# Kernel optimization log

Measured on AMD Instinct MI355X. Metric: run time of the kernel, lower is better.

The kernel has to match this reference:

```python
import jax, jax.numpy as jnp
import numpy as np

N = 50000      # nodes
F_IN = 1024    # raw feature dim
D = 64         # student_dim = hidden_dim * compression_ratio
P = 3          # number of meta-paths
E = 1600000    # edges per meta-path adjacency (avg degree 32)


def setup_inputs() -> dict:
    key = jax.random.key(0)
    ks = jax.random.split(key, 10)
    feats = jax.random.normal(ks[0], (N, F_IN), jnp.float32)
    rows = jax.random.randint(ks[1], (P, E), 0, N, dtype=jnp.int32)
    cols = jax.random.randint(ks[2], (P, E), 0, N, dtype=jnp.int32)
    # normalized-adjacency-like positive edge weights
    vals = jax.random.uniform(ks[3], (P, E), jnp.float32) / 32.0
    # fc_list[0]: Linear(F_IN -> D), xavier_normal gain=1.414
    W0 = jax.random.normal(ks[4], (D, F_IN), jnp.float32) * 0.05
    b0 = jnp.zeros((D,), jnp.float32)
    # P GCN linear layers (D -> D, no bias) + GCN bias params
    Wg = jax.random.normal(ks[5], (P, D, D), jnp.float32) * 0.17
    bg = jnp.zeros((P, D), jnp.float32)
    # PReLU alpha (torch default init 0.25, one scalar per GCN)
    alpha = jnp.full((P,), 0.25, jnp.float32)
    # Attention: Linear(D -> D) and att vector [1, D]
    Wa = jax.random.normal(ks[6], (D, D), jnp.float32) * 0.17
    ba = jnp.zeros((D,), jnp.float32)
    att = jax.random.normal(ks[7], (1, D), jnp.float32) * 0.17
    return dict(feats=feats, rows=rows, cols=cols, vals=vals, W0=W0, b0=b0,
                Wg=Wg, bg=bg, alpha=alpha, Wa=Wa, ba=ba, att=att)


def reference(feats, rows, cols, vals, W0, b0, Wg, bg, alpha, Wa, ba, att):
    # h = elu(fc_list[0](feats))  (feat_drop = 0 -> identity)
    h = jax.nn.elu(feats @ W0.T + b0)                       # [N, D]
    embeds = []
    for i in range(P):
        s = h @ Wg[i].T                                     # [N, D]
        # sparse adj (COO) @ s : out[r] += v * s[c]
        msg = vals[i][:, None] * s[cols[i]]                 # [E, D]
        out = jax.ops.segment_sum(msg, rows[i], num_segments=N)
        out = out + bg[i]
        embeds.append(jnp.where(out > 0, out, alpha[i] * out))  # PReLU
    emb = jnp.stack(embeds)                                 # [P, N, D]
    # Attention over views: beta_i = att . mean_n tanh(fc(emb_i))
    sp = jnp.tanh(jnp.einsum('pnd,ed->pne', emb, Wa) + ba).mean(axis=1)  # [P, D]
    beta = jax.nn.softmax(sp @ att[0])                      # [P]
    z_mp = jnp.einsum('p,pnd->nd', beta, emb)               # [N, D]
    return z_mp
```

## Files before the change

kernel.cpp:

```cpp
#include <hip/hip_runtime.h>
#include <hip/hip_bf16.h>

#define N_NODES 50000
#define F_IN    1024
#define DD      64
#define PP      3
#define EE      1600000
#define NPC     98
#define CCAP    17664

typedef __attribute__((ext_vector_type(8))) short short8v;
typedef __attribute__((ext_vector_type(4))) float floatx4;
typedef __attribute__((ext_vector_type(2))) float floatx2;

__device__ inline float bfl(uint u) { return __uint_as_float(u << 16); }
__device__ inline float bfh(uint u) { return __uint_as_float(u & 0xffff0000u); }
__device__ inline floatx2 up2(uint u) {
    floatx2 r; r.x = bfl(u); r.y = bfh(u); return r;
}
__device__ inline uint cvtpk2(float a, float b) {
    __hip_bfloat162 h = __float22bfloat162_rn(make_float2(a, b));
    return *(uint*)&h;
}
__device__ inline ushort f2bf(float x) {
    __hip_bfloat16 h = __float2bfloat16(x);
    return *(ushort*)&h;
}

__global__ __launch_bounds__(256) void split_weights(const float* __restrict__ W0,
                                                     const float* __restrict__ Wg,
                                                     ushort* __restrict__ W0h,
                                                     ushort* __restrict__ Wgh)
{
    int i = blockIdx.x * 256 + threadIdx.x;
    if (i < 64 * 1024) W0h[i] = f2bf(W0[i]);
    int j = i - 64 * 1024;
    if (j >= 0 && j < PP * 64 * 64) Wgh[j] = f2bf(Wg[j]);
}

__global__ __launch_bounds__(256) void gemm1_fused(const float* __restrict__ feats,
                                                   const ushort* __restrict__ W0h,
                                                   const float* __restrict__ b0,
                                                   const ushort* __restrict__ Wgh,
                                                   ushort* __restrict__ s_all)
{
    __shared__ ushort Ah[64 * 64];
    __shared__ ushort Bh[64 * 64];
    const int t = threadIdx.x;
    const int w = t >> 6, lane = t & 63;
    const int row0 = blockIdx.x * 64;
    const int l15 = lane & 15, l4 = lane >> 4;

    floatx4 acc[4] = {};

    for (int kc = 0; kc < 16; ++kc) {
        #pragma unroll
        for (int rep = 0; rep < 4; ++rep) {
            int idx = rep * 256 + t;
            int r = idx >> 4, c4 = idx & 15;
            int gr = row0 + r; if (gr >= N_NODES) gr = N_NODES - 1;
            float4 v = *(const float4*)&feats[(size_t)gr * F_IN + kc * 64 + c4 * 4];
            int unit = (c4 >> 1) ^ (r & 7);
            int base = r * 64 + unit * 8 + (c4 & 1) * 4;
            *(uint2*)&Ah[base] = make_uint2(cvtpk2(v.x, v.y), cvtpk2(v.z, v.w));
        }
        #pragma unroll
        for (int rep = 0; rep < 2; ++rep) {
            int idx = rep * 256 + t;
            int c = idx >> 3, u8 = idx & 7;
            uint4 vh = *(const uint4*)&W0h[(size_t)c * F_IN + kc * 64 + u8 * 8];
            int unit = u8 ^ (c & 7);
            *(uint4*)&Bh[c * 64 + unit * 8] = vh;
        }
        __syncthreads();
        #pragma unroll
        for (int ks = 0; ks < 2; ++ks) {
            int arow = w * 16 + l15;
            int au = (ks * 4 + l4) ^ (arow & 7);
            short8v ah = *(short8v*)&Ah[arow * 64 + au * 8];
            #pragma unroll
            for (int cf = 0; cf < 4; ++cf) {
                int bcol = cf * 16 + l15;
                int bu = (ks * 4 + l4) ^ (bcol & 7);
                short8v bh = *(short8v*)&Bh[bcol * 64 + bu * 8];
                acc[cf] = __builtin_amdgcn_mfma_f32_16x16x32_bf16(ah, bh, acc[cf], 0, 0, 0);
            }
        }
        __syncthreads();
    }

    #pragma unroll
    for (int cf = 0; cf < 4; ++cf) {
        int col = cf * 16 + l15;
        #pragma unroll
        for (int r = 0; r < 4; ++r) {
            int row = w * 16 + l4 * 4 + r;
            float x = acc[cf][r] + b0[col];
            x = x > 0.f ? x : (__expf(x) - 1.f);
            int u = (col >> 3) ^ (row & 7);
            Ah[row * 64 + u * 8 + (col & 7)] = f2bf(x);
        }
    }
    __syncthreads();

    for (int p = 0; p < PP; ++p) {
        #pragma unroll
        for (int rep = 0; rep < 2; ++rep) {
            int idx = rep * 256 + t;
            int r = idx >> 3, u8 = idx & 7;
            int unit = u8 ^ (r & 7);
            *(uint4*)&Bh[r * 64 + unit * 8] = *(const uint4*)&Wgh[(size_t)p * 4096 + idx * 8];
        }
        __syncthreads();

        floatx4 sacc[4] = {};
        #pragma unroll
        for (int ks = 0; ks < 2; ++ks) {
            int arow = w * 16 + l15;
            int au = (ks * 4 + l4) ^ (arow & 7);
            short8v ah = *(short8v*)&Ah[arow * 64 + au * 8];
            #pragma unroll
            for (int cf = 0; cf < 4; ++cf) {
                int bcol = cf * 16 + l15;
                int bu = (ks * 4 + l4) ^ (bcol & 7);
                short8v bh = *(short8v*)&Bh[bcol * 64 + bu * 8];
                sacc[cf] = __builtin_amdgcn_mfma_f32_16x16x32_bf16(ah, bh, sacc[cf], 0, 0, 0);
            }
        }
        ushort* sp = s_all + (size_t)p * N_NODES * 64;
        #pragma unroll
        for (int cf = 0; cf < 4; ++cf) {
            int col = cf * 16 + l15;
            #pragma unroll
            for (int r = 0; r < 4; ++r) {
                int gr = row0 + w * 16 + l4 * 4 + r;
                if (gr < N_NODES)
                    sp[(size_t)gr * 64 + col] = f2bf(sacc[cf][r]);
            }
        }
        __syncthreads();
    }
}

__global__ __launch_bounds__(256) void part1(const int*   __restrict__ rows,
                                             const int*   __restrict__ cols,
                                             const float* __restrict__ vals,
                                             int*   __restrict__ pcur3,
                                             uint2* __restrict__ coarsebuf)
{
    __shared__ uint2 stage[2560];
    __shared__ uint2 sorted[2560];
    __shared__ int cnt[128];
    __shared__ int sc[128];
    __shared__ int curb[128];
    __shared__ int gbase[128];
    const int t = threadIdx.x;
    const int path = blockIdx.y;
    const size_t ebase = (size_t)path * EE + (size_t)blockIdx.x * 2560;
    int* pcur = pcur3 + path * NPC;
    uint2* cb = coarsebuf + (size_t)path * NPC * CCAP;

    if (t < 128) { cnt[t] = 0; curb[t] = 0; }
    __syncthreads();

    #pragma unroll
    for (int it = 0; it < 10; ++it) {
        int e = it * 256 + t;
        int r = rows[ebase + e];
        int c = cols[ebase + e];
        float v = vals[ebase + e];
        int bin = r >> 9, rl = r & 511;
        stage[e] = make_uint2((uint)c | ((uint)rl << 16) | ((uint)bin << 25),
                              __float_as_uint(v));
        atomicAdd(&cnt[bin], 1);
    }
    __syncthreads();

    if (t < 128) sc[t] = cnt[t];
    __syncthreads();
    #pragma unroll
    for (int o = 1; o < 128; o <<= 1) {
        int v = (t < 128 && t >= o) ? sc[t - o] : 0;
        __syncthreads();
        if (t < 128 && t >= o) sc[t] += v;
        __syncthreads();
    }

    if (t < NPC) gbase[t] = atomicAdd(&pcur[t], cnt[t]);
    __syncthreads();

    #pragma unroll
    for (int it = 0; it < 10; ++it) {
        uint2 e = stage[it * 256 + t];
        int bin = e.x >> 25;
        int loc = (sc[bin] - cnt[bin]) + atomicAdd(&curb[bin], 1);
        sorted[loc] = e;
    }
    __syncthreads();

    #pragma unroll
    for (int it = 0; it < 10; ++it) {
        int i = it * 256 + t;
        uint2 e = sorted[i];
        int bin = e.x >> 25;
        int g = gbase[bin] + (i - (sc[bin] - cnt[bin]));
        if (g < CCAP) cb[(size_t)bin * CCAP + g] = e;
    }
}

__global__ __launch_bounds__(512) void sort2(const uint2* __restrict__ coarsebuf,
                                             const int*   __restrict__ pcur3,
                                             uint* __restrict__ sortpk,
                                             int* __restrict__ rowbeg3,
                                             int* __restrict__ rowend3)
{
    __shared__ int hist[512];
    __shared__ int cur[512];
    const int t = threadIdx.x;
    const int c = blockIdx.x, path = blockIdx.y;
    const int n = min(pcur3[path * NPC + c], CCAP);
    const size_t slabbase = ((size_t)path * NPC + c) * CCAP;
    const uint2* src = coarsebuf + slabbase;

    hist[t] = 0;
    __syncthreads();

    for (int i = t; i < n; i += 512)
        atomicAdd(&hist[(src[i].x >> 16) & 511], 1);
    __syncthreads();

    int c0 = hist[t];
    __syncthreads();
    #pragma unroll
    for (int o = 1; o < 512; o <<= 1) {
        int v = (t >= o) ? hist[t - o] : 0;
        __syncthreads();
        hist[t] += v;
        __syncthreads();
    }
    int excl = hist[t] - c0;
    cur[t] = excl;
    int gr = c * 512 + t;
    if (gr < N_NODES) {
        rowbeg3[path * N_NODES + gr] = (int)(slabbase + excl);
        rowend3[path * N_NODES + gr] = (int)(slabbase + excl + c0);
    }
    __syncthreads();

    for (int i = t; i < n; i += 512) {
        uint2 e = src[i];
        int rl = (e.x >> 16) & 511;
        int pos = atomicAdd(&cur[rl], 1);
        sortpk[slabbase + pos] = (e.x & 0xffffu) |
                                 ((uint)f2bf(__uint_as_float(e.y)) << 16);
    }
}

__global__ __launch_bounds__(256) void spmm_gather(const uint*   __restrict__ sortpk,
                                                   const int*    __restrict__ rowbeg3,
                                                   const int*    __restrict__ rowend3,
                                                   const ushort* __restrict__ s_all,
                                                   const float*  __restrict__ bg,
                                                   const float*  __restrict__ alpha,
                                                   ushort* __restrict__ emb)
{
    const int path = blockIdx.x / 12500;
    const int wid = (blockIdx.x % 12500) * 4 + (threadIdx.x >> 6);
    const int lane = threadIdx.x & 63;
    const int dq = lane & 7;
    const int slot = lane >> 3;
    const int e0 = rowbeg3[path * N_NODES + wid];
    const int e1 = rowend3[path * N_NODES + wid];
    const ushort* s_p = s_all + (size_t)path * N_NODES * 64;

    floatx2 acc[4] = {};
    if (e0 < e1) {
        const int last = e1 - 1;
        for (int e = e0; e < e1; e += 32) {
            int ea = e + slot, eb = ea + 8, ec = ea + 16, ed = ea + 24;
            uint pka = sortpk[min(ea, last)];
            uint pkb = sortpk[min(eb, last)];
            uint pkc = sortpk[min(ec, last)];
            uint pkd = sortpk[min(ed, last)];
            const uint4 ga = *(const uint4*)&s_p[(size_t)(pka & 0xffffu) * 64 + dq * 8];
            const uint4 gb = *(const uint4*)&s_p[(size_t)(pkb & 0xffffu) * 64 + dq * 8];
            const uint4 gc = *(const uint4*)&s_p[(size_t)(pkc & 0xffffu) * 64 + dq * 8];
            const uint4 gd = *(const uint4*)&s_p[(size_t)(pkd & 0xffffu) * 64 + dq * 8];
            float va = (ea <= last) ? bfh(pka) : 0.f;
            float vb = (eb <= last) ? bfh(pkb) : 0.f;
            float vc = (ec <= last) ? bfh(pkc) : 0.f;
            float vd = (ed <= last) ? bfh(pkd) : 0.f;
            floatx2 va2 = {va, va}, vb2 = {vb, vb}, vc2 = {vc, vc}, vd2 = {vd, vd};
            acc[0] += va2 * up2(ga.x); acc[1] += va2 * up2(ga.y);
            acc[2] += va2 * up2(ga.z); acc[3] += va2 * up2(ga.w);
            acc[0] += vb2 * up2(gb.x); acc[1] += vb2 * up2(gb.y);
            acc[2] += vb2 * up2(gb.z); acc[3] += vb2 * up2(gb.w);
            acc[0] += vc2 * up2(gc.x); acc[1] += vc2 * up2(gc.y);
            acc[2] += vc2 * up2(gc.z); acc[3] += vc2 * up2(gc.w);
            acc[0] += vd2 * up2(gd.x); acc[1] += vd2 * up2(gd.y);
            acc[2] += vd2 * up2(gd.z); acc[3] += vd2 * up2(gd.w);
        }
    }
    #pragma unroll
    for (int j = 0; j < 4; ++j) {
        acc[j].x += __shfl_xor(acc[j].x, 8);
        acc[j].y += __shfl_xor(acc[j].y, 8);
        acc[j].x += __shfl_xor(acc[j].x, 16);
        acc[j].y += __shfl_xor(acc[j].y, 16);
        acc[j].x += __shfl_xor(acc[j].x, 32);
        acc[j].y += __shfl_xor(acc[j].y, 32);
    }

    if (slot == 0) {
        const float al = alpha[path];
        const float* bgp = bg + path * 64;
        float x[8];
        #pragma unroll
        for (int j = 0; j < 4; ++j) {
            float v0 = acc[j].x + bgp[dq * 8 + 2 * j];
            float v1 = acc[j].y + bgp[dq * 8 + 2 * j + 1];
            x[2 * j]     = v0 > 0.f ? v0 : al * v0;
            x[2 * j + 1] = v1 > 0.f ? v1 : al * v1;
        }
        uint4 wv;
        wv.x = cvtpk2(x[0], x[1]);
        wv.y = cvtpk2(x[2], x[3]);
        wv.z = cvtpk2(x[4], x[5]);
        wv.w = cvtpk2(x[6], x[7]);
        *(uint4*)&emb[((size_t)path * N_NODES + wid) * 64 + dq * 8] = wv;
    }
}

__global__ __launch_bounds__(256) void postproc(const ushort* __restrict__ emb,
                                                const float* __restrict__ Wa,
                                                const float* __restrict__ ba,
                                                float* __restrict__ sp)
{
    __shared__ float Ws[64][64];
    __shared__ float As[64][64];
    __shared__ float red[16][64];
    const int t  = threadIdx.x;
    const int tx = t & 15;
    const int ty = t >> 4;
    const int nb = (N_NODES + 63) >> 6;
    const int p  = blockIdx.x / nb;
    const int tb = blockIdx.x % nb;
    const int row0 = tb * 64;
    const ushort* embp = emb + (size_t)p * N_NODES * 64;

    #pragma unroll
    for (int rep = 0; rep < 4; ++rep) {
        int id = rep * 1024 + t * 4;
        int e  = id >> 6;
        int k4 = id & 63;
        float4 wv = *(const float4*)&Wa[id];
        Ws[k4+0][e] = wv.x; Ws[k4+1][e] = wv.y;
        Ws[k4+2][e] = wv.z; Ws[k4+3][e] = wv.w;
    }
    #pragma unroll
    for (int rep = 0; rep < 2; ++rep) {
        int idx = rep * 256 + t;
        int m  = idx >> 3;
        int d8 = idx & 7;
        int gr = row0 + m;
        int gr2 = gr < N_NODES ? gr : N_NODES - 1;
        uint4 xv = *(const uint4*)&embp[(size_t)gr2 * 64 + d8 * 8];
        As[d8*8+0][m] = bfl(xv.x); As[d8*8+1][m] = bfh(xv.x);
        As[d8*8+2][m] = bfl(xv.y); As[d8*8+3][m] = bfh(xv.y);
        As[d8*8+4][m] = bfl(xv.z); As[d8*8+5][m] = bfh(xv.z);
        As[d8*8+6][m] = bfl(xv.w); As[d8*8+7][m] = bfh(xv.w);
    }
    __syncthreads();

    float acc[4][4] = {};
    #pragma unroll 8
    for (int kk = 0; kk < 64; ++kk) {
        float4 a4 = *(const float4*)&As[kk][ty * 4];
        float4 b4 = *(const float4*)&Ws[kk][tx * 4];
        float av[4] = {a4.x, a4.y, a4.z, a4.w};
        float bv[4] = {b4.x, b4.y, b4.z, b4.w};
        #pragma unroll
        for (int i = 0; i < 4; ++i)
            #pragma unroll
            for (int j = 0; j < 4; ++j)
                acc[i][j] += av[i] * bv[j];
    }

    float colsum[4] = {0.f, 0.f, 0.f, 0.f};
    #pragma unroll
    for (int i = 0; i < 4; ++i) {
        int gr = row0 + ty * 4 + i;
        if (gr < N_NODES) {
            #pragma unroll
            for (int j = 0; j < 4; ++j)
                colsum[j] += tanhf(acc[i][j] + ba[tx * 4 + j]);
        }
    }
    #pragma unroll
    for (int j = 0; j < 4; ++j) red[ty][tx * 4 + j] = colsum[j];
    __syncthreads();
    if (t < 64) {
        float ssum = 0.f;
        #pragma unroll
        for (int g = 0; g < 16; ++g) ssum += red[g][t];
        unsafeAtomicAdd(&sp[p * 64 + t], ssum);
    }
}

__global__ void beta_kernel(const float* __restrict__ sp,
                            const float* __restrict__ att,
                            float* __restrict__ beta)
{
    int lane = threadIdx.x;
    float w[PP];
    #pragma unroll
    for (int p = 0; p < PP; ++p) {
        float x = sp[p * 64 + lane] * (1.0f / (float)N_NODES) * att[lane];
        #pragma unroll
        for (int off = 32; off; off >>= 1) x += __shfl_down(x, off);
        w[p] = __shfl(x, 0);
    }
    if (lane == 0) {
        float mx = fmaxf(w[0], fmaxf(w[1], w[2]));
        float e0 = __expf(w[0] - mx);
        float e1 = __expf(w[1] - mx);
        float e2 = __expf(w[2] - mx);
        float s = e0 + e1 + e2;
        beta[0] = e0 / s; beta[1] = e1 / s; beta[2] = e2 / s;
    }
}

__global__ __launch_bounds__(256) void combine(const ushort* __restrict__ emb,
                                               const float* __restrict__ beta,
                                               float* __restrict__ out)
{
    const float b0 = beta[0], b1 = beta[1], b2 = beta[2];
    const size_t tot = (size_t)N_NODES * 64;
    size_t i = ((size_t)blockIdx.x * 256 + threadIdx.x) * 8;
    if (i < tot) {
        uint4 e0 = *(const uint4*)&emb[i];
        uint4 e1 = *(const uint4*)&emb[tot + i];
        uint4 e2 = *(const uint4*)&emb[2 * tot + i];
        float o[8];
        o[0] = b0*bfl(e0.x) + b1*bfl(e1.x) + b2*bfl(e2.x);
        o[1] = b0*bfh(e0.x) + b1*bfh(e1.x) + b2*bfh(e2.x);
        o[2] = b0*bfl(e0.y) + b1*bfl(e1.y) + b2*bfl(e2.y);
        o[3] = b0*bfh(e0.y) + b1*bfh(e1.y) + b2*bfh(e2.y);
        o[4] = b0*bfl(e0.z) + b1*bfl(e1.z) + b2*bfl(e2.z);
        o[5] = b0*bfh(e0.z) + b1*bfh(e1.z) + b2*bfh(e2.z);
        o[6] = b0*bfl(e0.w) + b1*bfl(e1.w) + b2*bfl(e2.w);
        o[7] = b0*bfh(e0.w) + b1*bfh(e1.w) + b2*bfh(e2.w);
        *(float4*)&out[i]     = make_float4(o[0], o[1], o[2], o[3]);
        *(float4*)&out[i + 4] = make_float4(o[4], o[5], o[6], o[7]);
    }
}

extern "C" void kernel_launch(void* const* d_in, const int* in_sizes, int n_in,
                              void* d_out, int out_size, void* d_ws, size_t ws_size,
                              hipStream_t stream)
{
    const float* feats = (const float*)d_in[0];
    const int*   rows  = (const int*)  d_in[1];
    const int*   cols  = (const int*)  d_in[2];
    const float* vals  = (const float*)d_in[3];
    const float* W0    = (const float*)d_in[4];
    const float* b0    = (const float*)d_in[5];
    const float* Wg    = (const float*)d_in[6];
    const float* bg    = (const float*)d_in[7];
    const float* alpha = (const float*)d_in[8];
    const float* Wa    = (const float*)d_in[9];
    const float* ba    = (const float*)d_in[10];
    const float* att   = (const float*)d_in[11];
    float* out = (float*)d_out;

    const size_t ND = (size_t)N_NODES * 64;
    char* base = (char*)d_ws;
    ushort* emb    = (ushort*)base;              base += 3 * ND * 2;
    ushort* s_all  = (ushort*)base;              base += 3 * ND * 2;
    ushort* W0h    = (ushort*)base;              base += 64 * 1024 * 2;
    ushort* Wgh    = (ushort*)base;              base += PP * 64 * 64 * 2;
    int*    pcur3  = (int*)base;                 base += PP * NPC * 4;
    float*  sp     = (float*)base;               base += 192 * 4;
    float*  beta   = (float*)base;               base += 64 * 4;
    int*    rowbeg3 = (int*)base;                base += PP * N_NODES * 4;
    int*    rowend3 = (int*)base;                base += PP * N_NODES * 4;
    base = (char*)(((size_t)base + 255) & ~(size_t)255);
    uint2*  coarsebuf = (uint2*)base;            base += (size_t)PP * NPC * CCAP * 8;
    uint*   sortpk    = (uint*)base;             base += (size_t)PP * NPC * CCAP * 4;

    hipMemsetAsync(pcur3, 0, (PP * NPC + 192) * sizeof(int), stream);

    split_weights<<<(64 * 1024 + PP * 64 * 64 + 255) / 256, 256, 0, stream>>>(
        W0, Wg, W0h, Wgh);

    gemm1_fused<<<782, 256, 0, stream>>>(feats, W0h, b0, Wgh, s_all);

    part1<<<dim3(EE / 2560, 3), 256, 0, stream>>>(rows, cols, vals, pcur3, coarsebuf);
    sort2<<<dim3(NPC, 3), 512, 0, stream>>>(coarsebuf, pcur3, sortpk, rowbeg3, rowend3);
    spmm_gather<<<3 * 12500, 256, 0, stream>>>(
        sortpk, rowbeg3, rowend3, s_all, bg, alpha, emb);

    postproc<<<3 * 782, 256, 0, stream>>>(emb, Wa, ba, sp);
    beta_kernel<<<1, 64, 0, stream>>>(sp, att, beta);
    combine<<<(int)((ND / 8 + 255) / 256), 256, 0, stream>>>(emb, beta, out);
}
```

Baseline: 313.4 us.

## Map eight rows per wave in SpMM gather and prefetch GEMM tiles into registers

The SpMM gather kernel now gives each wave eight rows, with one 8-lane group per row, instead of one row per wave. This removes the cross-lane shuffle reduction and cuts the block count, at the cost of divergence when rows in a wave have different degrees; the loop runs until every group is done. Separately, the first GEMM register-prefetches the next K-chunk of feats and W0 while the MFMAs run on the current one, overlapping global loads with compute at some register cost.

```diff
diff --git a/kernel.cpp b/kernel.cpp
--- a/kernel.cpp
+++ b/kernel.cpp
@@ -8,6 +8,7 @@
 #define EE      1600000
 #define NPC     98
 #define CCAP    17664
+#define RG      1563
 
 typedef __attribute__((ext_vector_type(8))) short short8v;
 typedef __attribute__((ext_vector_type(4))) float floatx4;
@@ -52,27 +53,58 @@
     const int l15 = lane & 15, l4 = lane >> 4;
 
     floatx4 acc[4] = {};
+    float4 pa[4];
+    uint4  pb[2];
+
+    #pragma unroll
+    for (int rep = 0; rep < 4; ++rep) {
+        int idx = rep * 256 + t;
+        int r = idx >> 4, c4 = idx & 15;
+        int gr = row0 + r; if (gr >= N_NODES) gr = N_NODES - 1;
+        pa[rep] = *(const float4*)&feats[(size_t)gr * F_IN + c4 * 4];
+    }
+    #pragma unroll
+    for (int rep = 0; rep < 2; ++rep) {
+        int idx = rep * 256 + t;
+        int c = idx >> 3, u8 = idx & 7;
+        pb[rep] = *(const uint4*)&W0h[(size_t)c * F_IN + u8 * 8];
+    }
 
     for (int kc = 0; kc < 16; ++kc) {
         #pragma unroll
         for (int rep = 0; rep < 4; ++rep) {
             int idx = rep * 256 + t;
             int r = idx >> 4, c4 = idx & 15;
-            int gr = row0 + r; if (gr >= N_NODES) gr = N_NODES - 1;
-            float4 v = *(const float4*)&feats[(size_t)gr * F_IN + kc * 64 + c4 * 4];
             int unit = (c4 >> 1) ^ (r & 7);
             int base = r * 64 + unit * 8 + (c4 & 1) * 4;
-            *(uint2*)&Ah[base] = make_uint2(cvtpk2(v.x, v.y), cvtpk2(v.z, v.w));
+            *(uint2*)&Ah[base] = make_uint2(cvtpk2(pa[rep].x, pa[rep].y),
+                                            cvtpk2(pa[rep].z, pa[rep].w));
         }
         #pragma unroll
         for (int rep = 0; rep < 2; ++rep) {
             int idx = rep * 256 + t;
             int c = idx >> 3, u8 = idx & 7;
-            uint4 vh = *(const uint4*)&W0h[(size_t)c * F_IN + kc * 64 + u8 * 8];
             int unit = u8 ^ (c & 7);
-            *(uint4*)&Bh[c * 64 + unit * 8] = vh;
-        }
-        __syncthreads();
+            *(uint4*)&Bh[c * 64 + unit * 8] = pb[rep];
+        }
+        __syncthreads();
+
+        if (kc < 15) {
+            #pragma unroll
+            for (int rep = 0; rep < 4; ++rep) {
+                int idx = rep * 256 + t;
+                int r = idx >> 4, c4 = idx & 15;
+                int gr = row0 + r; if (gr >= N_NODES) gr = N_NODES - 1;
+                pa[rep] = *(const float4*)&feats[(size_t)gr * F_IN + (kc + 1) * 64 + c4 * 4];
+            }
+            #pragma unroll
+            for (int rep = 0; rep < 2; ++rep) {
+                int idx = rep * 256 + t;
+                int c = idx >> 3, u8 = idx & 7;
+                pb[rep] = *(const uint4*)&W0h[(size_t)c * F_IN + (kc + 1) * 64 + u8 * 8];
+            }
+        }
+
         #pragma unroll
         for (int ks = 0; ks < 2; ++ks) {
             int arow = w * 16 + l15;
@@ -264,54 +296,49 @@
                                                    const float*  __restrict__ alpha,
                                                    ushort* __restrict__ emb)
 {
-    const int path = blockIdx.x / 12500;
-    const int wid = (blockIdx.x % 12500) * 4 + (threadIdx.x >> 6);
+    const int path = blockIdx.x / RG;
+    const int bi   = blockIdx.x % RG;
+    const int wv   = threadIdx.x >> 6;
     const int lane = threadIdx.x & 63;
-    const int dq = lane & 7;
-    const int slot = lane >> 3;
-    const int e0 = rowbeg3[path * N_NODES + wid];
-    const int e1 = rowend3[path * N_NODES + wid];
+    const int g    = lane >> 3;
+    const int dq   = lane & 7;
+    const int row  = (bi * 4 + wv) * 8 + g;
+    const int rowc = min(row, N_NODES - 1);
+    const int e0   = rowbeg3[path * N_NODES + rowc];
+    const int e1   = rowend3[path * N_NODES + rowc];
+    const int last = max(e1 - 1, 0);
     const ushort* s_p = s_all + (size_t)path * N_NODES * 64;
 
     floatx2 acc[4] = {};
-    if (e0 < e1) {
-        const int last = e1 - 1;
-        for (int e = e0; e < e1; e += 32) {
-            int ea = e + slot, eb = ea + 8, ec = ea + 16, ed = ea + 24;
-            uint pka = sortpk[min(ea, last)];
-            uint pkb = sortpk[min(eb, last)];
-            uint pkc = sortpk[min(ec, last)];
-            uint pkd = sortpk[min(ed, last)];
-            const uint4 ga = *(const uint4*)&s_p[(size_t)(pka & 0xffffu) * 64 + dq * 8];
-            const uint4 gb = *(const uint4*)&s_p[(size_t)(pkb & 0xffffu) * 64 + dq * 8];
-            const uint4 gc = *(const uint4*)&s_p[(size_t)(pkc & 0xffffu) * 64 + dq * 8];
-            const uint4 gd = *(const uint4*)&s_p[(size_t)(pkd & 0xffffu) * 64 + dq * 8];
-            float va = (ea <= last) ? bfh(pka) : 0.f;
-            float vb = (eb <= last) ? bfh(pkb) : 0.f;
-            float vc = (ec <= last) ? bfh(pkc) : 0.f;
-            float vd = (ed <= last) ? bfh(pkd) : 0.f;
-            floatx2 va2 = {va, va}, vb2 = {vb, vb}, vc2 = {vc, vc}, vd2 = {vd, vd};
-            acc[0] += va2 * up2(ga.x); acc[1] += va2 * up2(ga.y);
-            acc[2] += va2 * up2(ga.z); acc[3] += va2 * up2(ga.w);
-            acc[0] += vb2 * up2(gb.x); acc[1] += vb2 * up2(gb.y);
-            acc[2] += vb2 * up2(gb.z); acc[3] += vb2 * up2(gb.w);
-            acc[0] += vc2 * up2(gc.x); acc[1] += vc2 * up2(gc.y);
-            acc[2] += vc2 * up2(gc.z); acc[3] += vc2 * up2(gc.w);
-            acc[0] += vd2 * up2(gd.x); acc[1] += vd2 * up2(gd.y);
-            acc[2] += vd2 * up2(gd.z); acc[3] += vd2 * up2(gd.w);
-        }
-    }
-    #pragma unroll
-    for (int j = 0; j < 4; ++j) {
-        acc[j].x += __shfl_xor(acc[j].x, 8);
-        acc[j].y += __shfl_xor(acc[j].y, 8);
-        acc[j].x += __shfl_xor(acc[j].x, 16);
-        acc[j].y += __shfl_xor(acc[j].y, 16);
-        acc[j].x += __shfl_xor(acc[j].x, 32);
-        acc[j].y += __shfl_xor(acc[j].y, 32);
-    }
-
-    if (slot == 0) {
+    for (int e = e0; __any(e < e1); e += 4) {
+        int i0 = min(e,     last);
+        int i1 = min(e + 1, last);
+        int i2 = min(e + 2, last);
+        int i3 = min(e + 3, last);
+        uint pk0 = sortpk[i0];
+        uint pk1 = sortpk[i1];
+        uint pk2 = sortpk[i2];
+        uint pk3 = sortpk[i3];
+        const uint4 g0 = *(const uint4*)&s_p[(size_t)(pk0 & 0xffffu) * 64 + dq * 8];
+        const uint4 g1 = *(const uint4*)&s_p[(size_t)(pk1 & 0xffffu) * 64 + dq * 8];
+        const uint4 g2 = *(const uint4*)&s_p[(size_t)(pk2 & 0xffffu) * 64 + dq * 8];
+        const uint4 g3 = *(const uint4*)&s_p[(size_t)(pk3 & 0xffffu) * 64 + dq * 8];
+        float v0 = (e     < e1) ? bfh(pk0) : 0.f;
+        float v1 = (e + 1 < e1) ? bfh(pk1) : 0.f;
+        float v2 = (e + 2 < e1) ? bfh(pk2) : 0.f;
+        float v3 = (e + 3 < e1) ? bfh(pk3) : 0.f;
+        floatx2 v02 = {v0, v0}, v12 = {v1, v1}, v22 = {v2, v2}, v32 = {v3, v3};
+        acc[0] += v02 * up2(g0.x); acc[1] += v02 * up2(g0.y);
+        acc[2] += v02 * up2(g0.z); acc[3] += v02 * up2(g0.w);
+        acc[0] += v12 * up2(g1.x); acc[1] += v12 * up2(g1.y);
+        acc[2] += v12 * up2(g1.z); acc[3] += v12 * up2(g1.w);
+        acc[0] += v22 * up2(g2.x); acc[1] += v22 * up2(g2.y);
+        acc[2] += v22 * up2(g2.z); acc[3] += v22 * up2(g2.w);
+        acc[0] += v32 * up2(g3.x); acc[1] += v32 * up2(g3.y);
+        acc[2] += v32 * up2(g3.z); acc[3] += v32 * up2(g3.w);
+    }
+
+    if (row < N_NODES) {
         const float al = alpha[path];
         const float* bgp = bg + path * 64;
         float x[8];
@@ -322,12 +349,12 @@
             x[2 * j]     = v0 > 0.f ? v0 : al * v0;
             x[2 * j + 1] = v1 > 0.f ? v1 : al * v1;
         }
-        uint4 wv;
-        wv.x = cvtpk2(x[0], x[1]);
-        wv.y = cvtpk2(x[2], x[3]);
-        wv.z = cvtpk2(x[4], x[5]);
-        wv.w = cvtpk2(x[6], x[7]);
-        *(uint4*)&emb[((size_t)path * N_NODES + wid) * 64 + dq * 8] = wv;
+        uint4 wvv;
+        wvv.x = cvtpk2(x[0], x[1]);
+        wvv.y = cvtpk2(x[2], x[3]);
+        wvv.z = cvtpk2(x[4], x[5]);
+        wvv.w = cvtpk2(x[6], x[7]);
+        *(uint4*)&emb[((size_t)path * N_NODES + row) * 64 + dq * 8] = wvv;
     }
 }
 
@@ -497,7 +524,7 @@
 
     part1<<<dim3(EE / 2560, 3), 256, 0, stream>>>(rows, cols, vals, pcur3, coarsebuf);
     sort2<<<dim3(NPC, 3), 512, 0, stream>>>(coarsebuf, pcur3, sortpk, rowbeg3, rowend3);
-    spmm_gather<<<3 * 12500, 256, 0, stream>>>(
+    spmm_gather<<<3 * RG, 256, 0, stream>>>(
         sortpk, rowbeg3, rowend3, s_all, bg, alpha, emb);
 
     postproc<<<3 * 782, 256, 0, stream>>>(emb, Wa, ba, sp);
```

Measured after the change: 322.3 us. 1.03x slower.

## Prefetch next K-tile in gemm1 and move attention GEMM onto bf16 MFMA

Applied to the files above, without the earlier changes.

gemm1_fused now loads the next K-chunk of feats and W0 into registers before the MFMA work of the current chunk, so global-load latency overlaps compute. The postproc attention projection moves from a scalar fp32 outer-product loop to bf16 MFMA with swizzled LDS tiles, and Wa is pre-converted to bf16 in split_weights. Feeding Wa in bf16 lowers the precision of the tanh scores, and the register prefetch raises register pressure.

```diff
diff --git a/kernel.cpp b/kernel.cpp
--- a/kernel.cpp
+++ b/kernel.cpp
@@ -29,13 +29,17 @@
 
 __global__ __launch_bounds__(256) void split_weights(const float* __restrict__ W0,
                                                      const float* __restrict__ Wg,
+                                                     const float* __restrict__ Wa,
                                                      ushort* __restrict__ W0h,
-                                                     ushort* __restrict__ Wgh)
+                                                     ushort* __restrict__ Wgh,
+                                                     ushort* __restrict__ Wah)
 {
     int i = blockIdx.x * 256 + threadIdx.x;
     if (i < 64 * 1024) W0h[i] = f2bf(W0[i]);
     int j = i - 64 * 1024;
     if (j >= 0 && j < PP * 64 * 64) Wgh[j] = f2bf(Wg[j]);
+    int k = i - 64 * 1024 - PP * 64 * 64;
+    if (k >= 0 && k < 64 * 64) Wah[k] = f2bf(Wa[k]);
 }
 
 __global__ __launch_bounds__(256) void gemm1_fused(const float* __restrict__ feats,
@@ -52,27 +56,58 @@
     const int l15 = lane & 15, l4 = lane >> 4;
 
     floatx4 acc[4] = {};
+    float4 pa[4];
+    uint4  pb[2];
+
+    #pragma unroll
+    for (int rep = 0; rep < 4; ++rep) {
+        int idx = rep * 256 + t;
+        int r = idx >> 4, c4 = idx & 15;
+        int gr = row0 + r; if (gr >= N_NODES) gr = N_NODES - 1;
+        pa[rep] = *(const float4*)&feats[(size_t)gr * F_IN + c4 * 4];
+    }
+    #pragma unroll
+    for (int rep = 0; rep < 2; ++rep) {
+        int idx = rep * 256 + t;
+        int c = idx >> 3, u8 = idx & 7;
+        pb[rep] = *(const uint4*)&W0h[(size_t)c * F_IN + u8 * 8];
+    }
 
     for (int kc = 0; kc < 16; ++kc) {
         #pragma unroll
         for (int rep = 0; rep < 4; ++rep) {
             int idx = rep * 256 + t;
             int r = idx >> 4, c4 = idx & 15;
-            int gr = row0 + r; if (gr >= N_NODES) gr = N_NODES - 1;
-            float4 v = *(const float4*)&feats[(size_t)gr * F_IN + kc * 64 + c4 * 4];
             int unit = (c4 >> 1) ^ (r & 7);
             int base = r * 64 + unit * 8 + (c4 & 1) * 4;
-            *(uint2*)&Ah[base] = make_uint2(cvtpk2(v.x, v.y), cvtpk2(v.z, v.w));
+            *(uint2*)&Ah[base] = make_uint2(cvtpk2(pa[rep].x, pa[rep].y),
+                                            cvtpk2(pa[rep].z, pa[rep].w));
         }
         #pragma unroll
         for (int rep = 0; rep < 2; ++rep) {
             int idx = rep * 256 + t;
             int c = idx >> 3, u8 = idx & 7;
-            uint4 vh = *(const uint4*)&W0h[(size_t)c * F_IN + kc * 64 + u8 * 8];
             int unit = u8 ^ (c & 7);
-            *(uint4*)&Bh[c * 64 + unit * 8] = vh;
-        }
-        __syncthreads();
+            *(uint4*)&Bh[c * 64 + unit * 8] = pb[rep];
+        }
+        __syncthreads();
+
+        if (kc < 15) {
+            #pragma unroll
+            for (int rep = 0; rep < 4; ++rep) {
+                int idx = rep * 256 + t;
+                int r = idx >> 4, c4 = idx & 15;
+                int gr = row0 + r; if (gr >= N_NODES) gr = N_NODES - 1;
+                pa[rep] = *(const float4*)&feats[(size_t)gr * F_IN + (kc + 1) * 64 + c4 * 4];
+            }
+            #pragma unroll
+            for (int rep = 0; rep < 2; ++rep) {
+                int idx = rep * 256 + t;
+                int c = idx >> 3, u8 = idx & 7;
+                pb[rep] = *(const uint4*)&W0h[(size_t)c * F_IN + (kc + 1) * 64 + u8 * 8];
+            }
+        }
+
         #pragma unroll
         for (int ks = 0; ks < 2; ++ks) {
             int arow = w * 16 + l15;
@@ -332,16 +367,16 @@
 }
 
 __global__ __launch_bounds__(256) void postproc(const ushort* __restrict__ emb,
-                                                const float* __restrict__ Wa,
+                                                const ushort* __restrict__ Wah,
                                                 const float* __restrict__ ba,
                                                 float* __restrict__ sp)
 {
-    __shared__ float Ws[64][64];
-    __shared__ float As[64][64];
+    __shared__ ushort Ah[64 * 64];
+    __shared__ ushort Bh[64 * 64];
     __shared__ float red[16][64];
-    const int t  = threadIdx.x;
-    const int tx = t & 15;
-    const int ty = t >> 4;
+    const int t = threadIdx.x;
+    const int w = t >> 6, lane = t & 63;
+    const int l15 = lane & 15, l4 = lane >> 4;
     const int nb = (N_NODES + 63) >> 6;
     const int p  = blockIdx.x / nb;
     const int tb = blockIdx.x % nb;
@@ -349,55 +384,42 @@
     const ushort* embp = emb + (size_t)p * N_NODES * 64;
 
     #pragma unroll
-    for (int rep = 0; rep < 4; ++rep) {
-        int id = rep * 1024 + t * 4;
-        int e  = id >> 6;
-        int k4 = id & 63;
-        float4 wv = *(const float4*)&Wa[id];
-        Ws[k4+0][e] = wv.x; Ws[k4+1][e] = wv.y;
-        Ws[k4+2][e] = wv.z; Ws[k4+3][e] = wv.w;
-    }
-    #pragma unroll
     for (int rep = 0; rep < 2; ++rep) {
         int idx = rep * 256 + t;
-        int m  = idx >> 3;
-        int d8 = idx & 7;
-        int gr = row0 + m;
-        int gr2 = gr < N_NODES ? gr : N_NODES - 1;
-        uint4 xv = *(const uint4*)&embp[(size_t)gr2 * 64 + d8 * 8];
-        As[d8*8+0][m] = bfl(xv.x); As[d8*8+1][m] = bfh(xv.x);
-        As[d8*8+2][m] = bfl(xv.y); As[d8*8+3][m] = bfh(xv.y);
-        As[d8*8+4][m] = bfl(xv.z); As[d8*8+5][m] = bfh(xv.z);
-        As[d8*8+6][m] = bfl(xv.w); As[d8*8+7][m] = bfh(xv.w);
-    }
-    __syncthreads();
-
-    float acc[4][4] = {};
-    #pragma unroll 8
-    for (int kk = 0; kk < 64; ++kk) {
-        float4 a4 = *(const float4*)&As[kk][ty * 4];
-        float4 b4 = *(const float4*)&Ws[kk][tx * 4];
-        float av[4] = {a4.x, a4.y, a4.z, a4.w};
-        float bv[4] = {b4.x, b4.y, b4.z, b4.w};
-        #pragma unroll
-        for (int i = 0; i < 4; ++i)
-            #pragma unroll
-            for (int j = 0; j < 4; ++j)
-                acc[i][j] += av[i] * bv[j];
-    }
-
-    float colsum[4] = {0.f, 0.f, 0.f, 0.f};
-    #pragma unroll
-    for (int i = 0; i < 4; ++i) {
-        int gr = row0 + ty * 4 + i;
-        if (gr < N_NODES) {
-            #pragma unroll
-            for (int j = 0; j < 4; ++j)
-                colsum[j] += tanhf(acc[i][j] + ba[tx * 4 + j]);
-        }
-    }
-    #pragma unroll
-    for (int j = 0; j < 4; ++j) red[ty][tx * 4 + j] = colsum[j];
+        int r = idx >> 3, u8 = idx & 7;
+        int gr = row0 + r; if (gr >= N_NODES) gr = N_NODES - 1;
+        int unit = u8 ^ (r & 7);
+        *(uint4*)&Ah[r * 64 + unit * 8] = *(const uint4*)&embp[(size_t)gr * 64 + u8 * 8];
+        *(uint4*)&Bh[r * 64 + unit * 8] = *(const uint4*)&Wah[idx * 8];
+    }
+    __syncthreads();
+
+    floatx4 acc[4] = {};
+    #pragma unroll
+    for (int ks = 0; ks < 2; ++ks) {
+        int arow = w * 16 + l15;
+        int au = (ks * 4 + l4) ^ (arow & 7);
+        short8v ah = *(short8v*)&Ah[arow * 64 + au * 8];
+        #pragma unroll
+        for (int cf = 0; cf < 4; ++cf) {
+            int bcol = cf * 16 + l15;
+            int bu = (ks * 4 + l4) ^ (bcol & 7);
+            short8v bh = *(short8v*)&Bh[bcol * 64 + bu * 8];
+            acc[cf] = __builtin_amdgcn_mfma_f32_16x16x32_bf16(ah, bh, acc[cf], 0, 0, 0);
+        }
+    }
+
+    #pragma unroll
+    for (int cf = 0; cf < 4; ++cf) {
+        int col = cf * 16 + l15;
+        float s = 0.f;
+        #pragma unroll
+        for (int r = 0; r < 4; ++r) {
+            int gr = row0 + w * 16 + l4 * 4 + r;
+            if (gr < N_NODES) s += tanhf(acc[cf][r] + ba[col]);
+        }
+        red[w * 4 + l4][col] = s;
+    }
     __syncthreads();
     if (t < 64) {
         float ssum = 0.f;
@@ -479,6 +501,7 @@
     ushort* s_all  = (ushort*)base;              base += 3 * ND * 2;
     ushort* W0h    = (ushort*)base;              base += 64 * 1024 * 2;
     ushort* Wgh    = (ushort*)base;              base += PP * 64 * 64 * 2;
+    ushort* Wah    = (ushort*)base;              base += 64 * 64 * 2;
     int*    pcur3  = (int*)base;                 base += PP * NPC * 4;
     float*  sp     = (float*)base;               base += 192 * 4;
     float*  beta   = (float*)base;               base += 64 * 4;
@@ -490,8 +513,8 @@
 
     hipMemsetAsync(pcur3, 0, (PP * NPC + 192) * sizeof(int), stream);
 
-    split_weights<<<(64 * 1024 + PP * 64 * 64 + 255) / 256, 256, 0, stream>>>(
-        W0, Wg, W0h, Wgh);
+    split_weights<<<(64 * 1024 + PP * 64 * 64 + 64 * 64 + 255) / 256, 256, 0, stream>>>(
+        W0, Wg, Wa, W0h, Wgh, Wah);
 
     gemm1_fused<<<782, 256, 0, stream>>>(feats, W0h, b0, Wgh, s_all);
 
@@ -500,7 +523,7 @@
     spmm_gather<<<3 * 12500, 256, 0, stream>>>(
         sortpk, rowbeg3, rowend3, s_all, bg, alpha, emb);
 
-    postproc<<<3 * 782, 256, 0, stream>>>(emb, Wa, ba, sp);
+    postproc<<<3 * 782, 256, 0, stream>>>(emb, Wah, ba, sp);
     beta_kernel<<<1, 64, 0, stream>>>(sp, att, beta);
     combine<<<(int)((ND / 8 + 255) / 256), 256, 0, stream>>>(emb, beta, out);
 }
```

New measurement: 316.8 us. Within noise of the previous version (+1.1%).
